# Kernel tuning notes

Measured on AMD Instinct MI355X. Metric: run time of the kernel, lower is better.

## Reference

```python
import jax, jax.numpy as jnp
import numpy as np

N_NODES = 50000
N_EDGES = 800000
D = 128
BN_EPS = 1e-5

def setup_inputs() -> dict:
    key = jax.random.key(0)
    k1, k2, k3, k4, k5 = jax.random.split(key, 5)
    features = jax.random.normal(k1, (N_NODES, D), dtype=jnp.float32)
    W = jax.random.normal(k2, (D, D), dtype=jnp.float32) * (1.0 / np.sqrt(D))
    b = jax.random.normal(k3, (D,), dtype=jnp.float32) * 0.01
    gamma = jnp.ones((D,), dtype=jnp.float32)
    beta = jnp.zeros((D,), dtype=jnp.float32)
    edge_src = jax.random.randint(k4, (N_EDGES,), 0, N_NODES, dtype=jnp.int32)
    edge_dst = jax.random.randint(k5, (N_EDGES,), 0, N_NODES, dtype=jnp.int32)
    return {"features": features, "W": W, "b": b, "gamma": gamma,
            "beta": beta, "edge_src": edge_src, "edge_dst": edge_dst}

def reference(features, W, b, gamma, beta, edge_src, edge_dst):
    h_in = features
    # in-degrees per node, clamped to >= 1
    degs = jax.ops.segment_sum(jnp.ones_like(edge_dst, dtype=jnp.float32),
                               edge_dst, num_segments=N_NODES)
    norm = jnp.clip(degs, 1.0, None) ** -0.5  # [N]
    norm = norm[:, None]                       # [N, 1]
    # symmetric-norm GCN: scale, copy_src + sum reduce, linear apply, scale
    x = features * norm
    agg = jax.ops.segment_sum(x[edge_src], edge_dst, num_segments=N_NODES)  # [N, D]
    h = agg @ W.T + b
    h = h * norm
    # BatchNorm1d (training-mode math: batch stats over nodes, biased var)
    mean = jnp.mean(h, axis=0)
    var = jnp.mean((h - mean) ** 2, axis=0)
    h = (h - mean) * jax.lax.rsqrt(var + BN_EPS) * gamma + beta
    # ReLU activation, residual; dropout is identity in eval
    h = jax.nn.relu(h)
    h = h_in + h
    return h
```

## Files before the change

### kernel.cpp

```cpp
#include <hip/hip_runtime.h>

#define D 128
#define BN_EPS 1e-5f
#define NPART 8
#define NCHUNK 256
#define CAP 64
#define NBKT 16

typedef __attribute__((ext_vector_type(8))) short short8;
typedef __attribute__((ext_vector_type(4))) float f32x4;

__device__ __forceinline__ unsigned short f2bf(float f) {
    unsigned int x = __float_as_uint(f);
    return (unsigned short)((x + 0x7fffu + ((x >> 16) & 1u)) >> 16);
}

__device__ __forceinline__ void atomAddF(float* p, float v) {
    unsafeAtomicAdd(p, v);
}

__global__ __launch_bounds__(256) void k_prep(
        const int* __restrict__ src, const int* __restrict__ dst,
        int* __restrict__ cnt, unsigned short* __restrict__ srcs,
        int nE, int PS, int CH,
        const float4* __restrict__ inA, ushort4* __restrict__ outA, int n4a,
        const float4* __restrict__ inB, ushort4* __restrict__ outB, int n4b) {
    int bid = blockIdx.x;
    if (bid < NPART * NCHUNK) {
        int p = bid & (NPART - 1);
        int c = bid >> 3;
        unsigned lo = (unsigned)(p * PS);
        int e0 = c * CH;
        int e1 = min(e0 + CH, nE);
        for (int e = e0 + (int)threadIdx.x; e < e1; e += 2048) {
            int dd[8]; bool aa[8]; int ss[8];
            #pragma unroll
            for (int t = 0; t < 8; ++t) {
                int idx = e + t * 256;
                bool in = idx < e1;
                int d = in ? dst[idx] : 0;
                dd[t] = d;
                aa[t] = in && ((unsigned)d - lo < (unsigned)PS);
            }
            #pragma unroll
            for (int t = 0; t < 8; ++t)
                ss[t] = aa[t] ? atomicAdd(&cnt[dd[t]], 1) : CAP;
            #pragma unroll
            for (int t = 0; t < 8; ++t)
                if (ss[t] < CAP)
                    srcs[(size_t)dd[t] * CAP + ss[t]] = (unsigned short)src[e + t * 256];
        }
    } else {
        int i = (bid - NPART * NCHUNK) * 256 + threadIdx.x;
        const float4* in; ushort4* out; int k;
        if (i < n4a) { in = inA; out = outA; k = i; }
        else { k = i - n4a; if (k >= n4b) return; in = inB; out = outB; }
        float4 v = in[k];
        ushort4 o;
        o.x = f2bf(v.x); o.y = f2bf(v.y); o.z = f2bf(v.z); o.w = f2bf(v.w);
        out[k] = o;
    }
}

template <bool FB>
__global__ __launch_bounds__(256, 2) void k_gg(
        const int* __restrict__ cnt,
        const unsigned short* __restrict__ srcs,
        const void* __restrict__ featp,
        const unsigned short* __restrict__ Wbf,
        const float* __restrict__ b,
        float* __restrict__ h,
        float* __restrict__ colpart,
        int nN) {
    __shared__ unsigned short Ald[64 * 136];
    __shared__ float tp[4][16 * 36];

    const int tid = threadIdx.x;
    const int row0 = blockIdx.x * 64;

    {
        const int hw = tid >> 5;
        const int l = tid & 31;
        for (int j = 0; j < 8; ++j) {
            int local = hw * 8 + j;
            int node = row0 + local;
            float a0 = 0.0f, a1 = 0.0f, a2 = 0.0f, a3 = 0.0f;
            if (node < nN) {
                int end = cnt[node];
                if (end > CAP) end = CAP;
                const unsigned short* sl = srcs + (size_t)node * CAP;
                int i = 0;
                if (FB) {
                    const uint2* fb = (const uint2*)featp + l;
                    for (; i + 7 < end; i += 8) {
                        int s[8];
                        #pragma unroll
                        for (int t = 0; t < 8; ++t) s[t] = sl[i + t];
                        uint2 u[8];
                        #pragma unroll
                        for (int t = 0; t < 8; ++t) u[t] = fb[(size_t)s[t] * 32];
                        float nm[8];
                        #pragma unroll
                        for (int t = 0; t < 8; ++t)
                            nm[t] = rsqrtf(fmaxf((float)cnt[s[t]], 1.0f));
                        #pragma unroll
                        for (int t = 0; t < 8; ++t) {
                            a0 += __uint_as_float(u[t].x << 16) * nm[t];
                            a1 += __uint_as_float(u[t].x & 0xffff0000u) * nm[t];
                            a2 += __uint_as_float(u[t].y << 16) * nm[t];
                            a3 += __uint_as_float(u[t].y & 0xffff0000u) * nm[t];
                        }
                    }
                    for (; i < end; ++i) {
                        int s = sl[i];
                        float nm = rsqrtf(fmaxf((float)cnt[s], 1.0f));
                        uint2 u = fb[(size_t)s * 32];
                        a0 += __uint_as_float(u.x << 16) * nm;
                        a1 += __uint_as_float(u.x & 0xffff0000u) * nm;
                        a2 += __uint_as_float(u.y << 16) * nm;
                        a3 += __uint_as_float(u.y & 0xffff0000u) * nm;
                    }
                } else {
                    const float4* fb = (const float4*)featp + l;
                    for (; i + 3 < end; i += 4) {
                        int s0 = sl[i], s1 = sl[i + 1], s2 = sl[i + 2], s3 = sl[i + 3];
                        float n0 = rsqrtf(fmaxf((float)cnt[s0], 1.0f));
                        float n1 = rsqrtf(fmaxf((float)cnt[s1], 1.0f));
                        float n2 = rsqrtf(fmaxf((float)cnt[s2], 1.0f));
                        float n3 = rsqrtf(fmaxf((float)cnt[s3], 1.0f));
                        float4 f0 = fb[(size_t)s0 * 32], f1 = fb[(size_t)s1 * 32];
                        float4 f2 = fb[(size_t)s2 * 32], f3 = fb[(size_t)s3 * 32];
                        a0 += f0.x * n0 + f1.x * n1 + f2.x * n2 + f3.x * n3;
                        a1 += f0.y * n0 + f1.y * n1 + f2.y * n2 + f3.y * n3;
                        a2 += f0.z * n0 + f1.z * n1 + f2.z * n2 + f3.z * n3;
                        a3 += f0.w * n0 + f1.w * n1 + f2.w * n2 + f3.w * n3;
                    }
                    for (; i < end; ++i) {
                        int s = sl[i];
                        float nm = rsqrtf(fmaxf((float)cnt[s], 1.0f));
                        float4 f = fb[(size_t)s * 32];
                        a0 += f.x * nm; a1 += f.y * nm; a2 += f.z * nm; a3 += f.w * nm;
                    }
                }
            }
            uint2 packed;
            packed.x = (unsigned int)f2bf(a0) | ((unsigned int)f2bf(a1) << 16);
            packed.y = (unsigned int)f2bf(a2) | ((unsigned int)f2bf(a3) << 16);
            *(uint2*)&Ald[local * 136 + l * 4] = packed;
        }
    }
    __syncthreads();

    const int lane = tid & 63;
    const int wv = tid >> 6;
    const int wcol0 = wv * 32;
    const int l15 = lane & 15;
    const int lq = lane >> 4;

    short8 bfrag[2][4];
    #pragma unroll
    for (int ct = 0; ct < 2; ++ct) {
        int n = wcol0 + ct * 16 + l15;
        #pragma unroll
        for (int kc = 0; kc < 4; ++kc)
            bfrag[ct][kc] = *(const short8*)(Wbf + n * 128 + kc * 32 + lq * 8);
    }
    const float bc0 = b[wcol0 + l15], bc1 = b[wcol0 + 16 + l15];

    float s1[2] = {0.0f, 0.0f}, s2[2] = {0.0f, 0.0f};
    const int sub = lane & 3;
    const int r16 = lane >> 2;

    #pragma unroll
    for (int rt = 0; rt < 4; ++rt) {
        int r0 = row0 + rt * 16;
        short8 af[4];
        #pragma unroll
        for (int kc = 0; kc < 4; ++kc)
            af[kc] = *(const short8*)(Ald + (rt * 16 + l15) * 136 + kc * 32 + lq * 8);

        f32x4 acc0 = {0.0f, 0.0f, 0.0f, 0.0f};
        f32x4 acc1 = {0.0f, 0.0f, 0.0f, 0.0f};
        #pragma unroll
        for (int kc = 0; kc < 4; ++kc) {
            acc0 = __builtin_amdgcn_mfma_f32_16x16x32_bf16(af[kc], bfrag[0][kc], acc0, 0, 0, 0);
            acc1 = __builtin_amdgcn_mfma_f32_16x16x32_bf16(af[kc], bfrag[1][kc], acc1, 0, 0, 0);
        }

        #pragma unroll
        for (int reg = 0; reg < 4; ++reg) {
            int row = r0 + lq * 4 + reg;
            float nm = 0.0f;
            if (row < nN) nm = rsqrtf(fmaxf((float)cnt[row], 1.0f));
            float v0 = (acc0[reg] + bc0) * nm;
            float v1 = (acc1[reg] + bc1) * nm;
            int lrow = lq * 4 + reg;
            tp[wv][lrow * 36 + l15]      = v0;
            tp[wv][lrow * 36 + 16 + l15] = v1;
            if (row < nN) {
                s1[0] += v0; s2[0] += v0 * v0;
                s1[1] += v1; s2[1] += v1 * v1;
            }
        }
        int row = r0 + r16;
        if (row < nN) {
            float4 t0 = *(const float4*)&tp[wv][r16 * 36 + sub * 4];
            float4 t1 = *(const float4*)&tp[wv][r16 * 36 + 16 + sub * 4];
            size_t base = (size_t)row * 128 + wcol0 + sub * 4;
            *(float4*)(h + base) = t0;
            *(float4*)(h + base + 16) = t1;
        }
    }

    #pragma unroll
    for (int ct = 0; ct < 2; ++ct) {
        s1[ct] += __shfl_xor(s1[ct], 16, 64);
        s1[ct] += __shfl_xor(s1[ct], 32, 64);
        s2[ct] += __shfl_xor(s2[ct], 16, 64);
        s2[ct] += __shfl_xor(s2[ct], 32, 64);
    }
    const int bkt = blockIdx.x & (NBKT - 1);
    if (lane < 16) {
        atomAddF(&colpart[(wcol0 + lane) * NBKT + bkt], s1[0]);
        atomAddF(&colpart[(128 + wcol0 + lane) * NBKT + bkt], s2[0]);
        atomAddF(&colpart[(wcol0 + 16 + lane) * NBKT + bkt], s1[1]);
        atomAddF(&colpart[(128 + wcol0 + 16 + lane) * NBKT + bkt], s2[1]);
    }
}

__global__ __launch_bounds__(256) void k_bn_out(const float* __restrict__ colpart,
                                                const float* __restrict__ gamma,
                                                const float* __restrict__ beta,
                                                float* __restrict__ h,
                                                const float* __restrict__ feat,
                                                float inv_n, int total4) {
    __shared__ float sc[128], sh[128];
    int tid = threadIdx.x;
    if (tid < 128) {
        float s = 0.0f, q = 0.0f;
        #pragma unroll
        for (int j = 0; j < NBKT; ++j) {
            s += colpart[tid * NBKT + j];
            q += colpart[(128 + tid) * NBKT + j];
        }
        float mean = s * inv_n;
        float var = q * inv_n - mean * mean;
        float scv = gamma[tid] * rsqrtf(var + BN_EPS);
        sc[tid] = scv;
        sh[tid] = beta[tid] - mean * scv;
    }
    __syncthreads();
    int t = blockIdx.x * 256 + tid;
    if (t >= total4) return;
    int base = t * 4;
    int j = base & 127;
    float4 hv = *(const float4*)(h + base);
    float4 fv = *(const float4*)(feat + base);
    float4 o;
    o.x = fv.x + fmaxf(hv.x * sc[j + 0] + sh[j + 0], 0.0f);
    o.y = fv.y + fmaxf(hv.y * sc[j + 1] + sh[j + 1], 0.0f);
    o.z = fv.z + fmaxf(hv.z * sc[j + 2] + sh[j + 2], 0.0f);
    o.w = fv.w + fmaxf(hv.w * sc[j + 3] + sh[j + 3], 0.0f);
    *(float4*)(h + base) = o;
}

extern "C" void kernel_launch(void* const* d_in, const int* in_sizes, int n_in,
                              void* d_out, int out_size, void* d_ws, size_t ws_size,
                              hipStream_t stream) {
    const float* feat  = (const float*)d_in[0];
    const float* W     = (const float*)d_in[1];
    const float* b     = (const float*)d_in[2];
    const float* gamma = (const float*)d_in[3];
    const float* beta  = (const float*)d_in[4];
    const int* esrc = (const int*)d_in[5];
    const int* edst = (const int*)d_in[6];

    const int nN = in_sizes[0] / D;
    const int nE = in_sizes[5];
    const int PS = (nN + NPART - 1) / NPART;
    const int CH = (nE + NCHUNK - 1) / NCHUNK;

    float* h = (float*)d_out;

    unsigned short* Wbf    = (unsigned short*)d_ws;
    unsigned short* srcs   = Wbf + 128 * 128;
    int*            cnt    = (int*)(srcs + (size_t)nN * CAP);
    float*          colpart= (float*)(cnt + nN);
    unsigned short* featbf = (unsigned short*)(colpart + 256 * NBKT);

    size_t need_full = (size_t)((char*)(featbf + (size_t)nN * D) - (char*)d_ws);
    bool useFB = ws_size >= need_full;

    hipMemsetAsync(cnt, 0, ((size_t)nN + 256 * NBKT + 64) * sizeof(int), stream);

    int n4a = 128 * 128 / 4;
    int n4b = useFB ? nN * D / 4 : 0;
    int castBlocks = (n4a + n4b + 255) / 256;
    k_prep<<<NPART * NCHUNK + castBlocks, 256, 0, stream>>>(
        esrc, edst, cnt, srcs, nE, PS, CH,
        (const float4*)W, (ushort4*)Wbf, n4a,
        (const float4*)feat, (ushort4*)featbf, n4b);

    int gb = (nN + 63) / 64;
    if (useFB)
        k_gg<true><<<gb, 256, 0, stream>>>(cnt, srcs, featbf, Wbf, b, h, colpart, nN);
    else
        k_gg<false><<<gb, 256, 0, stream>>>(cnt, srcs, feat, Wbf, b, h, colpart, nN);

    int total4 = nN * D / 4;
    float inv_n = 1.0f / (float)nN;
    k_bn_out<<<(total4 + 255) / 256, 256, 0, stream>>>(colpart, gamma, beta,
                                                       h, feat, inv_n, total4);
}
```

Measured before the change: 214.0 us.

## Split fused gather+GEMM kernel into separate gather and MFMA GEMM kernels

Splits the fused kernel into two. The first is a gather kernel that assigns one 32-lane group per node and writes the bf16 aggregates to a global workspace buffer. The second is a GEMM kernel that reads those aggregates straight from global memory into MFMA fragments. This removes the per-block serial gather of 64 nodes and the shared-memory staging, so the gather can use full-GPU parallelism and occupancy without the GEMM's register pressure. In exchange it adds an extra global round trip of the aggregate buffer and one more kernel launch. When the workspace is too small, it falls back to using the output buffer as scratch.

After: 211.2 us. No clear change (-1.3%).

```diff
diff --git a/kernel.cpp b/kernel.cpp
--- a/kernel.cpp
+++ b/kernel.cpp
@@ -63,99 +63,100 @@
 }
 
 template <bool FB>
-__global__ __launch_bounds__(256, 2) void k_gg(
-        const int* __restrict__ cnt,
-        const unsigned short* __restrict__ srcs,
-        const void* __restrict__ featp,
+__global__ __launch_bounds__(256) void k_gather(const int* __restrict__ cnt,
+                                                const unsigned short* __restrict__ srcs,
+                                                const void* __restrict__ featp,
+                                                uint2* __restrict__ aggout,
+                                                int strideU2, int offU2,
+                                                int nN) {
+    int node = (blockIdx.x * 256 + threadIdx.x) >> 5;
+    if (node >= nN) return;
+    int l = threadIdx.x & 31;
+
+    int end = cnt[node];
+    if (end > CAP) end = CAP;
+    const unsigned short* sl = srcs + (size_t)node * CAP;
+
+    float a0 = 0.0f, a1 = 0.0f, a2 = 0.0f, a3 = 0.0f;
+    int i = 0;
+
+    if (FB) {
+        const uint2* fb = (const uint2*)featp + l;
+        for (; i + 7 < end; i += 8) {
+            int s[8];
+            #pragma unroll
+            for (int t = 0; t < 8; ++t) s[t] = sl[i + t];
+            uint2 u[8];
+            #pragma unroll
+            for (int t = 0; t < 8; ++t) u[t] = fb[(size_t)s[t] * 32];
+            float nm[8];
+            #pragma unroll
+            for (int t = 0; t < 8; ++t)
+                nm[t] = rsqrtf(fmaxf((float)cnt[s[t]], 1.0f));
+            #pragma unroll
+            for (int t = 0; t < 8; ++t) {
+                a0 += __uint_as_float(u[t].x << 16) * nm[t];
+                a1 += __uint_as_float(u[t].x & 0xffff0000u) * nm[t];
+                a2 += __uint_as_float(u[t].y << 16) * nm[t];
+                a3 += __uint_as_float(u[t].y & 0xffff0000u) * nm[t];
+            }
+        }
+        for (; i < end; ++i) {
+            int s = sl[i];
+            float nm = rsqrtf(fmaxf((float)cnt[s], 1.0f));
+            uint2 u = fb[(size_t)s * 32];
+            a0 += __uint_as_float(u.x << 16) * nm;
+            a1 += __uint_as_float(u.x & 0xffff0000u) * nm;
+            a2 += __uint_as_float(u.y << 16) * nm;
+            a3 += __uint_as_float(u.y & 0xffff0000u) * nm;
+        }
+    } else {
+        const float4* fb = (const float4*)featp + l;
+        for (; i + 3 < end; i += 4) {
+            int s0 = sl[i], s1 = sl[i + 1], s2 = sl[i + 2], s3 = sl[i + 3];
+            float n0 = rsqrtf(fmaxf((float)cnt[s0], 1.0f));
+            float n1 = rsqrtf(fmaxf((float)cnt[s1], 1.0f));
+            float n2 = rsqrtf(fmaxf((float)cnt[s2], 1.0f));
+            float n3 = rsqrtf(fmaxf((float)cnt[s3], 1.0f));
+            float4 f0 = fb[(size_t)s0 * 32], f1 = fb[(size_t)s1 * 32];
+            float4 f2 = fb[(size_t)s2 * 32], f3 = fb[(size_t)s3 * 32];
+            a0 += f0.x * n0 + f1.x * n1 + f2.x * n2 + f3.x * n3;
+            a1 += f0.y * n0 + f1.y * n1 + f2.y * n2 + f3.y * n3;
+            a2 += f0.z * n0 + f1.z * n1 + f2.z * n2 + f3.z * n3;
+            a3 += f0.w * n0 + f1.w * n1 + f2.w * n2 + f3.w * n3;
+        }
+        for (; i < end; ++i) {
+            int s = sl[i];
+            float nm = rsqrtf(fmaxf((float)cnt[s], 1.0f));
+            float4 f = fb[(size_t)s * 32];
+            a0 += f.x * nm; a1 += f.y * nm; a2 += f.z * nm; a3 += f.w * nm;
+        }
+    }
+    uint2 packed;
+    packed.x = (unsigned int)f2bf(a0) | ((unsigned int)f2bf(a1) << 16);
+    packed.y = (unsigned int)f2bf(a2) | ((unsigned int)f2bf(a3) << 16);
+    aggout[(size_t)node * strideU2 + offU2 + l] = packed;
+}
+
+template <bool SAFE>
+__global__ __launch_bounds__(256) void k_gemm(
+        const unsigned short* __restrict__ Adata,
+        int strideS, int offS,
         const unsigned short* __restrict__ Wbf,
         const float* __restrict__ b,
+        const int* __restrict__ cnt,
         float* __restrict__ h,
         float* __restrict__ colpart,
         int nN) {
-    __shared__ unsigned short Ald[64 * 136];
-    __shared__ float tp[4][16 * 36];
-
     const int tid = threadIdx.x;
-    const int row0 = blockIdx.x * 64;
-
-    {
-        const int hw = tid >> 5;
-        const int l = tid & 31;
-        for (int j = 0; j < 8; ++j) {
-            int local = hw * 8 + j;
-            int node = row0 + local;
-            float a0 = 0.0f, a1 = 0.0f, a2 = 0.0f, a3 = 0.0f;
-            if (node < nN) {
-                int end = cnt[node];
-                if (end > CAP) end = CAP;
-                const unsigned short* sl = srcs + (size_t)node * CAP;
-                int i = 0;
-                if (FB) {
-                    const uint2* fb = (const uint2*)featp + l;
-                    for (; i + 7 < end; i += 8) {
-                        int s[8];
-                        #pragma unroll
-                        for (int t = 0; t < 8; ++t) s[t] = sl[i + t];
-                        uint2 u[8];
-                        #pragma unroll
-                        for (int t = 0; t < 8; ++t) u[t] = fb[(size_t)s[t] * 32];
-                        float nm[8];
-                        #pragma unroll
-                        for (int t = 0; t < 8; ++t)
-                            nm[t] = rsqrtf(fmaxf((float)cnt[s[t]], 1.0f));
-                        #pragma unroll
-                        for (int t = 0; t < 8; ++t) {
-                            a0 += __uint_as_float(u[t].x << 16) * nm[t];
-                            a1 += __uint_as_float(u[t].x & 0xffff0000u) * nm[t];
-                            a2 += __uint_as_float(u[t].y << 16) * nm[t];
-                            a3 += __uint_as_float(u[t].y & 0xffff0000u) * nm[t];
-                        }
-                    }
-                    for (; i < end; ++i) {
-                        int s = sl[i];
-                        float nm = rsqrtf(fmaxf((float)cnt[s], 1.0f));
-                        uint2 u = fb[(size_t)s * 32];
-                        a0 += __uint_as_float(u.x << 16) * nm;
-                        a1 += __uint_as_float(u.x & 0xffff0000u) * nm;
-                        a2 += __uint_as_float(u.y << 16) * nm;
-                        a3 += __uint_as_float(u.y & 0xffff0000u) * nm;
-                    }
-                } else {
-                    const float4* fb = (const float4*)featp + l;
-                    for (; i + 3 < end; i += 4) {
-                        int s0 = sl[i], s1 = sl[i + 1], s2 = sl[i + 2], s3 = sl[i + 3];
-                        float n0 = rsqrtf(fmaxf((float)cnt[s0], 1.0f));
-                        float n1 = rsqrtf(fmaxf((float)cnt[s1], 1.0f));
-                        float n2 = rsqrtf(fmaxf((float)cnt[s2], 1.0f));
-                        float n3 = rsqrtf(fmaxf((float)cnt[s3], 1.0f));
-                        float4 f0 = fb[(size_t)s0 * 32], f1 = fb[(size_t)s1 * 32];
-                        float4 f2 = fb[(size_t)s2 * 32], f3 = fb[(size_t)s3 * 32];
-                        a0 += f0.x * n0 + f1.x * n1 + f2.x * n2 + f3.x * n3;
-                        a1 += f0.y * n0 + f1.y * n1 + f2.y * n2 + f3.y * n3;
-                        a2 += f0.z * n0 + f1.z * n1 + f2.z * n2 + f3.z * n3;
-                        a3 += f0.w * n0 + f1.w * n1 + f2.w * n2 + f3.w * n3;
-                    }
-                    for (; i < end; ++i) {
-                        int s = sl[i];
-                        float nm = rsqrtf(fmaxf((float)cnt[s], 1.0f));
-                        float4 f = fb[(size_t)s * 32];
-                        a0 += f.x * nm; a1 += f.y * nm; a2 += f.z * nm; a3 += f.w * nm;
-                    }
-                }
-            }
-            uint2 packed;
-            packed.x = (unsigned int)f2bf(a0) | ((unsigned int)f2bf(a1) << 16);
-            packed.y = (unsigned int)f2bf(a2) | ((unsigned int)f2bf(a3) << 16);
-            *(uint2*)&Ald[local * 136 + l * 4] = packed;
-        }
-    }
-    __syncthreads();
-
     const int lane = tid & 63;
     const int wv = tid >> 6;
     const int wcol0 = wv * 32;
     const int l15 = lane & 15;
     const int lq = lane >> 4;
+    const int row0 = blockIdx.x * 64;
+
+    __shared__ float tp[4][16 * 36];
 
     short8 bfrag[2][4];
     #pragma unroll
@@ -167,6 +168,19 @@
     }
     const float bc0 = b[wcol0 + l15], bc1 = b[wcol0 + 16 + l15];
 
+    short8 apre[4][4];
+    if (SAFE) {
+        #pragma unroll
+        for (int rt = 0; rt < 4; ++rt) {
+            int arow = row0 + rt * 16 + l15;
+            int arc = arow < nN ? arow : (nN - 1);
+            #pragma unroll
+            for (int kc = 0; kc < 4; ++kc)
+                apre[rt][kc] = *(const short8*)(Adata + (size_t)arc * strideS + offS + kc * 32 + lq * 8);
+        }
+        __syncthreads();
+    }
+
     float s1[2] = {0.0f, 0.0f}, s2[2] = {0.0f, 0.0f};
     const int sub = lane & 3;
     const int r16 = lane >> 2;
@@ -175,9 +189,16 @@
     for (int rt = 0; rt < 4; ++rt) {
         int r0 = row0 + rt * 16;
         short8 af[4];
-        #pragma unroll
-        for (int kc = 0; kc < 4; ++kc)
-            af[kc] = *(const short8*)(Ald + (rt * 16 + l15) * 136 + kc * 32 + lq * 8);
+        if (SAFE) {
+            #pragma unroll
+            for (int kc = 0; kc < 4; ++kc) af[kc] = apre[rt][kc];
+        } else {
+            int arow = r0 + l15;
+            int arc = arow < nN ? arow : (nN - 1);
+            #pragma unroll
+            for (int kc = 0; kc < 4; ++kc)
+                af[kc] = *(const short8*)(Adata + (size_t)arc * strideS + offS + kc * 32 + lq * 8);
+        }
 
         f32x4 acc0 = {0.0f, 0.0f, 0.0f, 0.0f};
         f32x4 acc1 = {0.0f, 0.0f, 0.0f, 0.0f};
@@ -286,10 +307,13 @@
     unsigned short* srcs   = Wbf + 128 * 128;
     int*            cnt    = (int*)(srcs + (size_t)nN * CAP);
     float*          colpart= (float*)(cnt + nN);
-    unsigned short* featbf = (unsigned short*)(colpart + 256 * NBKT);
-
+    unsigned short* aggbuf = (unsigned short*)(colpart + 256 * NBKT);
+    unsigned short* featbf = aggbuf + (size_t)nN * D;
+
+    size_t need_agg  = (size_t)((char*)(aggbuf + (size_t)nN * D) - (char*)d_ws);
     size_t need_full = (size_t)((char*)(featbf + (size_t)nN * D) - (char*)d_ws);
-    bool useFB = ws_size >= need_full;
+    bool useAgg = ws_size >= need_agg;
+    bool useFB  = ws_size >= need_full;
 
     hipMemsetAsync(cnt, 0, ((size_t)nN + 256 * NBKT + 64) * sizeof(int), stream);
 
@@ -301,11 +325,22 @@
         (const float4*)W, (ushort4*)Wbf, n4a,
         (const float4*)feat, (ushort4*)featbf, n4b);
 
+    uint2* aggdst = useAgg ? (uint2*)aggbuf : (uint2*)d_out;
+    int strideU2 = useAgg ? 32 : 64;
+    int offU2    = useAgg ? 0  : 32;
+
+    int gblocks = (nN * 32 + 255) / 256;
+    if (useFB)
+        k_gather<true><<<gblocks, 256, 0, stream>>>(cnt, srcs, featbf, aggdst, strideU2, offU2, nN);
+    else
+        k_gather<false><<<gblocks, 256, 0, stream>>>(cnt, srcs, feat, aggdst, strideU2, offU2, nN);
+
     int gb = (nN + 63) / 64;
-    if (useFB)
-        k_gg<true><<<gb, 256, 0, stream>>>(cnt, srcs, featbf, Wbf, b, h, colpart, nN);
+    if (useAgg)
+        k_gemm<false><<<gb, 256, 0, stream>>>(aggbuf, 128, 0, Wbf, b, cnt, h, colpart, nN);
     else
-        k_gg<false><<<gb, 256, 0, stream>>>(cnt, srcs, feat, Wbf, b, h, colpart, nN);
+        k_gemm<true><<<gb, 256, 0, stream>>>((const unsigned short*)d_out, 256, 128,
+                                             Wbf, b, cnt, h, colpart, nN);
 
     int total4 = nN * D / 4;
     float inv_n = 1.0f / (float)nN;
```
